# Kernel tuning notes

Hardware: AMD Instinct MI355X
Metric: run time of the kernel (lower is better)

Reference implementation:

```python
import jax, jax.numpy as jnp
import numpy as np

B = 128          # graphs per batch
NPG = 512        # nodes per graph
N = B * NPG      # 65536 nodes
E = 262144       # edges, avg degree 4, intra-graph only
IN_FEATS = 128
EDGE_FEATS = 32
EMB = 64
HEADS = 4
HC = EMB * HEADS  # 256
L = 3


def setup_inputs():
    ki = iter(jax.random.split(jax.random.key(0), 64))

    def nrm(shape):
        return jax.random.normal(next(ki), shape, jnp.float32)

    def lin(fan_in, shape):
        return jax.random.uniform(next(ki), shape, jnp.float32, -1.0, 1.0) / np.float32(np.sqrt(fan_in))

    x = nrm((N, IN_FEATS))
    edge_attr = nrm((E, EDGE_FEATS))
    g = jnp.arange(E) // (E // B)  # each edge stays inside its graph
    src = g * NPG + jax.random.randint(next(ki), (E,), 0, NPG)
    dst = g * NPG + jax.random.randint(next(ki), (E,), 0, NPG)
    edge_index = jnp.stack([src, dst]).astype(jnp.int32)
    batch_index = (jnp.arange(N) // NPG).astype(jnp.int32)
    d = dict(x=x, edge_attr=edge_attr, edge_index=edge_index, batch_index=batch_index)
    d['Wq1'] = lin(IN_FEATS, (IN_FEATS, HC)); d['bq1'] = lin(IN_FEATS, (HC,))
    d['Wk1'] = lin(IN_FEATS, (IN_FEATS, HC)); d['bk1'] = lin(IN_FEATS, (HC,))
    d['Wv1'] = lin(IN_FEATS, (IN_FEATS, HC)); d['bv1'] = lin(IN_FEATS, (HC,))
    d['We1'] = lin(EDGE_FEATS, (EDGE_FEATS, HC))
    d['Wskip1'] = lin(IN_FEATS, (IN_FEATS, HC)); d['bskip1'] = lin(IN_FEATS, (HC,))
    d['Wbeta1'] = lin(3 * HC, (3 * HC,))
    d['Wt1'] = lin(HC, (HC, EMB)); d['bt1'] = lin(HC, (EMB,))
    d['bng1'] = jnp.ones((EMB,), jnp.float32); d['bnb1'] = jnp.zeros((EMB,), jnp.float32)
    d['Wq'] = lin(EMB, (L, EMB, HC)); d['bq'] = lin(EMB, (L, HC))
    d['Wk'] = lin(EMB, (L, EMB, HC)); d['bk'] = lin(EMB, (L, HC))
    d['Wv'] = lin(EMB, (L, EMB, HC)); d['bv'] = lin(EMB, (L, HC))
    d['We'] = lin(EDGE_FEATS, (L, EDGE_FEATS, HC))
    d['Wskip'] = lin(EMB, (L, EMB, HC)); d['bskip'] = lin(EMB, (L, HC))
    d['Wbeta'] = lin(3 * HC, (L, 3 * HC))
    d['Wt'] = lin(HC, (L, HC, EMB)); d['bt'] = lin(HC, (L, EMB))
    d['bng'] = jnp.ones((L, EMB), jnp.float32); d['bnb'] = jnp.zeros((L, EMB), jnp.float32)
    d['pw0'] = lin(EMB, (EMB,)); d['pw2'] = lin(EMB, (EMB,))
    return d


def _tconv(x, src, dst, eattr, emask, Wq, bq, Wk, bk, Wv, bv, We, Wskip, bskip, Wbeta, n):
    # PyG TransformerConv (concat=True, beta=True, edge_dim), dropout off (eval)
    q = (x @ Wq + bq).reshape(n, HEADS, EMB)
    k = (x @ Wk + bk).reshape(n, HEADS, EMB)
    v = (x @ Wv + bv).reshape(n, HEADS, EMB)
    e = (eattr @ We).reshape(-1, HEADS, EMB)
    alpha = jnp.einsum('ehc,ehc->eh', q[dst], k[src] + e) / (EMB ** 0.5)
    alpha = jnp.where(emask[:, None], alpha, -jnp.inf)
    m = jax.ops.segment_max(alpha, dst, num_segments=n)
    m = jnp.where(jnp.isfinite(m), m, 0.0)
    p = jnp.where(emask[:, None], jnp.exp(alpha - m[dst]), 0.0)
    den = jax.ops.segment_sum(p, dst, num_segments=n)
    p = p / jnp.maximum(den, 1e-16)[dst]
    out = jax.ops.segment_sum((v[src] + e) * p[:, :, None], dst, num_segments=n).reshape(n, HC)
    xr = x @ Wskip + bskip
    beta = jax.nn.sigmoid(jnp.concatenate([out, xr, out - xr], axis=-1) @ Wbeta)[:, None]
    return beta * xr + (1.0 - beta) * out


def _bn(x, g, b):
    mu = x.mean(0)
    var = jnp.mean((x - mu) ** 2, 0)
    return (x - mu) / jnp.sqrt(var + 1e-5) * g + b


def _topk(x, src, dst, emask, w, npg, k_keep):
    # PyG TopKPooling: score = tanh(x.w / |w|), keep top ratio per graph, scale kept x by score
    n_graphs = x.shape[0] // npg
    score = jnp.tanh((x @ w) / jnp.linalg.norm(w))
    sv, idx = jax.lax.top_k(score.reshape(n_graphs, npg), k_keep)
    perm = (idx + jnp.arange(n_graphs)[:, None] * npg).reshape(-1)
    x_new = x[perm] * sv.reshape(-1)[:, None]
    new_idx = jnp.full(n_graphs * npg, -1, jnp.int32).at[perm].set(
        jnp.arange(n_graphs * k_keep, dtype=jnp.int32))
    sn, dn = new_idx[src], new_idx[dst]
    valid = emask & (sn >= 0) & (dn >= 0)
    return x_new, jnp.where(valid, sn, 0), jnp.where(valid, dn, 0), valid


def _forward(x, edge_attr, edge_index, batch_index, Wq1, bq1, Wk1, bk1, Wv1, bv1,
             We1, Wskip1, bskip1, Wbeta1, Wt1, bt1, bng1, bnb1,
             Wq, bq, Wk, bk, Wv, bv, We, Wskip, bskip, Wbeta, Wt, bt, bng, bnb,
             pw0, pw2):
    src, dst = edge_index[0], edge_index[1]
    emask = jnp.ones(src.shape, dtype=bool)
    n = x.shape[0]
    npg = n // B
    x = _tconv(x, src, dst, edge_attr, emask, Wq1, bq1, Wk1, bk1, Wv1, bv1,
               We1, Wskip1, bskip1, Wbeta1, n)
    x = _bn(jax.nn.relu(x @ Wt1 + bt1), bng1, bnb1)
    pool_w = {0: pw0, 2: pw2}
    greps = []
    for i in range(L):
        x = _tconv(x, src, dst, edge_attr, emask, Wq[i], bq[i], Wk[i], bk[i], Wv[i], bv[i],
                   We[i], Wskip[i], bskip[i], Wbeta[i], n)
        x = _bn(jax.nn.relu(x @ Wt[i] + bt[i]), bng[i], bnb[i])
        if i % 3 == 0 or i == L - 1:  # pooling at layers 0 and 2
            k_keep = npg // 2
            x, src, dst, emask = _topk(x, src, dst, emask, pool_w[i], npg, k_keep)
            npg = k_keep
            n = B * npg
            batch = jnp.arange(n) // npg  # pooled nodes stay contiguous per graph
            gmax = jax.ops.segment_max(x, batch, num_segments=B)
            gmean = jax.ops.segment_sum(x, batch, num_segments=B) / npg
            greps.append(jnp.concatenate([gmax, gmean], axis=-1))
    return greps[0] + greps[1]


def reference(x, edge_attr, edge_index, batch_index, Wq1, bq1, Wk1, bk1, Wv1, bv1,
              We1, Wskip1, bskip1, Wbeta1, Wt1, bt1, bng1, bnb1,
              Wq, bq, Wk, bk, Wv, bv, We, Wskip, bskip, Wbeta, Wt, bt, bng, bnb,
              pw0, pw2):
    return _forward(x, edge_attr, edge_index, batch_index, Wq1, bq1, Wk1, bk1, Wv1, bv1,
                    We1, Wskip1, bskip1, Wbeta1, Wt1, bt1, bng1, bnb1,
                    Wq, bq, Wk, bk, Wv, bv, We, Wskip, bskip, Wbeta, Wt, bt, bng, bnb,
                    pw0, pw2)
```

## Files before the change

### kernel.cpp

```cpp
#include <hip/hip_runtime.h>
#include <hip/hip_bf16.h>

#define NGRAPH 128
#define NTOT   65536
#define NE     262144
#define EPG    2048
#define HC     256

typedef __hip_bfloat16 bf16;

__device__ __forceinline__ float4 f4fma(float a, float4 b, float4 c){
  return make_float4(fmaf(a,b.x,c.x), fmaf(a,b.y,c.y), fmaf(a,b.z,c.z), fmaf(a,b.w,c.w));
}
__device__ __forceinline__ float4 f4add(float4 a, float4 b){
  return make_float4(a.x+b.x, a.y+b.y, a.z+b.z, a.w+b.w);
}

template<int F>
__global__ __launch_bounds__(256)
void gemm_qkvs_kernel(const float* __restrict__ X,
                      const float* __restrict__ W0, const float* __restrict__ B0,
                      const float* __restrict__ W1, const float* __restrict__ B1,
                      const float* __restrict__ W2, const float* __restrict__ B2,
                      const float* __restrict__ W3, const float* __restrict__ B3,
                      float* __restrict__ Y, long ystride)
{
  const int s = blockIdx.y;
  const float* __restrict__ W = (s==0)?W0:(s==1)?W1:(s==2)?W2:W3;
  const float* __restrict__ Bb= (s==0)?B0:(s==1)?B1:(s==2)?B2:B3;
  float* __restrict__ Yo = Y + (long)s*ystride;

  __shared__ __align__(16) float XsT[F][36];
  const int tid  = threadIdx.x;
  const int tcol = tid & 63;
  const int trow = tid >> 6;
  const long r0 = (long)blockIdx.x * 32;
  for (int idx = tid; idx < 32*F; idx += 256){
    int r = idx / F;
    int f = idx - r*F;
    XsT[f][r] = X[(r0 + r)*F + f];
  }
  __syncthreads();
  float4 acc[8];
#pragma unroll
  for (int r = 0; r < 8; ++r) acc[r] = make_float4(0.f,0.f,0.f,0.f);
  for (int f = 0; f < F; ++f){
    float4 w = *(const float4*)(&W[f*HC + 4*tcol]);
    float xs[8];
    *(float4*)&xs[0] = *(const float4*)(&XsT[f][8*trow]);
    *(float4*)&xs[4] = *(const float4*)(&XsT[f][8*trow + 4]);
#pragma unroll
    for (int r = 0; r < 8; ++r) acc[r] = f4fma(xs[r], w, acc[r]);
  }
  float4 bb = *(const float4*)(&Bb[4*tcol]);
#pragma unroll
  for (int r = 0; r < 8; ++r)
    *(float4*)(&Yo[(r0 + 8*trow + r)*HC + 4*tcol]) = f4add(acc[r], bb);
}

__global__ void mcomb_kernel(const float* __restrict__ Wq,
                             const float* __restrict__ bq,
                             const float* __restrict__ We,
                             int F, float* __restrict__ M)
{
  int id = blockIdx.x*256 + threadIdx.x;
  if (id >= (F+1)*128) return;
  int g = id >> 7;
  int j = id & 127;
  int h = j >> 5, f = j & 31;
  const float* row = (g < F) ? (Wq + (long)g*HC) : bq;
  const float* wr  = We + (long)f*HC + h*64;
  float s = 0.f;
#pragma unroll
  for (int c = 0; c < 64; ++c) s = fmaf(row[h*64 + c], wr[c], s);
  M[id] = s;
}

template<int F>
__global__ __launch_bounds__(256)
void qwe_gemm_kernel(const float* __restrict__ X, const float* __restrict__ M,
                     float* __restrict__ qwe)
{
  __shared__ __align__(16) float XsT[F][68];
  const int tid  = threadIdx.x;
  const int tcol = tid & 31;
  const int trow = tid >> 5;
  const long r0 = (long)blockIdx.x * 64;
  for (int idx = tid; idx < 64*F; idx += 256){
    int r = idx / F;
    int f = idx - r*F;
    XsT[f][r] = X[(r0 + r)*F + f];
  }
  __syncthreads();
  float4 acc[8];
#pragma unroll
  for (int r = 0; r < 8; ++r) acc[r] = make_float4(0.f,0.f,0.f,0.f);
  for (int f = 0; f < F; ++f){
    float4 w = *(const float4*)(&M[f*128 + 4*tcol]);
    float xs[8];
    *(float4*)&xs[0] = *(const float4*)(&XsT[f][8*trow]);
    *(float4*)&xs[4] = *(const float4*)(&XsT[f][8*trow + 4]);
#pragma unroll
    for (int r = 0; r < 8; ++r) acc[r] = f4fma(xs[r], w, acc[r]);
  }
  float4 bb = *(const float4*)(&M[F*128 + 4*tcol]);
#pragma unroll
  for (int r = 0; r < 8; ++r)
    *(float4*)(&qwe[(r0 + 8*trow + r)*128 + 4*tcol]) = f4add(acc[r], bb);
}

__global__ __launch_bounds__(256)
void csr_build_kernel(const int* __restrict__ dstA, int npgLoc,
                      int* __restrict__ eids, int* __restrict__ rowptr,
                      int* __restrict__ deg)
{
  __shared__ int dloc[2048];
  __shared__ int ord[2048];
  __shared__ int cnt[512];
  __shared__ int base[512];
  const int g = blockIdx.x, tid = threadIdx.x;
  const int ebase = g*2048;
  const int nbase = g*npgLoc;
  for (int e = tid; e < 2048; e += 256){
    int d = dstA[ebase + e];
    dloc[e] = (d >= 0) ? (d - nbase) : -1;
  }
  for (int d = tid; d < npgLoc; d += 256) cnt[d] = 0;
  __syncthreads();
  for (int r = 0; r < 8; ++r){
    const int e = r*256 + tid;
    const int d = dloc[e];
    int rk = -1;
    if (d >= 0){
      rk = cnt[d];
      for (int u = r*256; u < e; ++u)
        rk += (dloc[u] == d);
    }
    ord[e] = rk;
    __syncthreads();
    if (d >= 0) atomicAdd(&cnt[d], 1);
    __syncthreads();
  }
  if (tid == 0){
    int run = 0;
    for (int d = 0; d < npgLoc; ++d){ base[d] = run; run += cnt[d]; }
  }
  __syncthreads();
  for (int e = tid; e < 2048; e += 256){
    int d = dloc[e];
    if (d >= 0) eids[ebase + base[d] + ord[e]] = ebase + e;
  }
  for (int d = tid; d < npgLoc; d += 256){
    rowptr[nbase + d] = ebase + base[d];
    deg   [nbase + d] = cnt[d];
  }
}

__global__ __launch_bounds__(256)
void attn_kernel(int nodeOff,
                 const float* q, const float* __restrict__ k,
                 const float* __restrict__ v, const float* __restrict__ skip,
                 const float* __restrict__ qwe,
                 const int* __restrict__ rowptr, const int* __restrict__ deg,
                 const int* __restrict__ eids, const int* __restrict__ srcA,
                 const float* __restrict__ EA, const float* __restrict__ We,
                 const float* __restrict__ Wb, float* xout)
{
  const int lane = threadIdx.x & 63;
  const int h    = threadIdx.x >> 6;
  const int il   = blockIdx.x;
  const int i    = nodeOff + il;
  const int c    = h*64 + lane;

  const float qv = q[(long)il*HC + c];
  const float qw = (lane < 32) ? qwe[(long)il*128 + h*32 + lane] : 0.f;

  const int p0 = rowptr[i];
  const int dg = deg[i];
  int e_l = 0, s_l = 0;
  if (lane < dg){ e_l = eids[p0 + lane]; s_l = srcA[e_l] - nodeOff; }

  float m = -__builtin_inff();
  float den = 0.f, acc = 0.f, wsum = 0.f;

  for (int t = 0; t < dg; ++t){
    int e, s;
    if (t < 64){ e = __shfl(e_l, t); s = __shfl(s_l, t); }
    else { e = eids[p0 + t]; s = srcA[e] - nodeOff; }
    float ea = (lane < 32) ? EA[(long)e*32 + lane] : 0.f;
    float kk = k[(long)s*HC + c];
    float vv = v[(long)s*HC + c];
    float part = fmaf(qv, kk, ea*qw);
    part += __shfl_xor(part, 1);
    part += __shfl_xor(part, 2);
    part += __shfl_xor(part, 4);
    part += __shfl_xor(part, 8);
    part += __shfl_xor(part, 16);
    part += __shfl_xor(part, 32);
    float alpha = part * 0.125f;
    float nm  = fmaxf(m, alpha);
    float scl = __expf(m - nm);
    float p   = __expf(alpha - nm);
    den  = den*scl + p;
    acc  = fmaf(acc,  scl, p*vv);
    wsum = fmaf(wsum, scl, p*ea);
    m = nm;
  }

  float ecorr = 0.f;
#pragma unroll
  for (int f = 0; f < 32; ++f)
    ecorr = fmaf(__shfl(wsum, f), We[f*HC + c], ecorr);
  float inv = 1.f / fmaxf(den, 1e-16f);
  float o = (acc + ecorr) * inv;

  float xr = skip[(long)il*HC + c];
  float tp = o*Wb[c] + xr*Wb[HC + c] + (o - xr)*Wb[2*HC + c];
  tp += __shfl_xor(tp, 1);
  tp += __shfl_xor(tp, 2);
  tp += __shfl_xor(tp, 4);
  tp += __shfl_xor(tp, 8);
  tp += __shfl_xor(tp, 16);
  tp += __shfl_xor(tp, 32);
  __shared__ float tsh[4];
  if (lane == 0) tsh[h] = tp;
  __syncthreads();
  float tt = tsh[0] + tsh[1] + tsh[2] + tsh[3];
  float beta = 1.f / (1.f + __expf(-tt));
  xout[(long)il*HC + c] = beta*xr + (1.f - beta)*o;
}

__global__ __launch_bounds__(256)
void gemm_wt_kernel(const float* __restrict__ Xa, const float* __restrict__ Wt,
                    const float* __restrict__ bt, float* __restrict__ y)
{
  __shared__ __align__(16) float XsT[64][132];
  const int tid  = threadIdx.x;
  const int tcol = tid & 15;
  const int trow = tid >> 4;
  const long r0 = (long)blockIdx.x * 128;
  float4 acc[8];
#pragma unroll
  for (int r = 0; r < 8; ++r) acc[r] = make_float4(0.f,0.f,0.f,0.f);
  for (int kc = 0; kc < 4; ++kc){
    for (int idx = tid; idx < 128*64; idx += 256){
      int r = idx >> 6;
      int f = idx & 63;
      XsT[f][r] = Xa[(r0 + r)*HC + kc*64 + f];
    }
    __syncthreads();
    for (int f = 0; f < 64; ++f){
      float4 w = *(const float4*)(&Wt[(kc*64 + f)*64 + 4*tcol]);
      float xs[8];
      *(float4*)&xs[0] = *(const float4*)(&XsT[f][8*trow]);
      *(float4*)&xs[4] = *(const float4*)(&XsT[f][8*trow + 4]);
#pragma unroll
      for (int r = 0; r < 8; ++r) acc[r] = f4fma(xs[r], w, acc[r]);
    }
    __syncthreads();
  }
  float4 bb = *(const float4*)(&bt[4*tcol]);
#pragma unroll
  for (int r = 0; r < 8; ++r){
    float4 o = f4add(acc[r], bb);
    o.x = fmaxf(o.x, 0.f); o.y = fmaxf(o.y, 0.f);
    o.z = fmaxf(o.z, 0.f); o.w = fmaxf(o.w, 0.f);
    *(float4*)(&y[(r0 + 8*trow + r)*64 + 4*tcol]) = o;
  }
}

__global__ __launch_bounds__(256)
void bn_stats_kernel(const float* __restrict__ y, long total4,
                     float* __restrict__ psum, float* __restrict__ psq)
{
  __shared__ float s1[256][4], s2[256][4];
  const int tid = threadIdx.x;
  float a0=0,a1=0,a2=0,a3=0,b0=0,b1=0,b2=0,b3=0;
  const float4* y4 = (const float4*)y;
  for (long j = (long)blockIdx.x*256 + tid; j < total4; j += 65536){
    float4 v = y4[j];
    a0 += v.x; b0 += v.x*v.x;
    a1 += v.y; b1 += v.y*v.y;
    a2 += v.z; b2 += v.z*v.z;
    a3 += v.w; b3 += v.w*v.w;
  }
  s1[tid][0]=a0; s1[tid][1]=a1; s1[tid][2]=a2; s1[tid][3]=a3;
  s2[tid][0]=b0; s2[tid][1]=b1; s2[tid][2]=b2; s2[tid][3]=b3;
  __syncthreads();
  if (tid < 64){
    int t0 = tid >> 2, comp = tid & 3;
    float sa = 0.f, sb = 0.f;
#pragma unroll
    for (int kk = 0; kk < 16; ++kk){
      sa += s1[t0 + 16*kk][comp];
      sb += s2[t0 + 16*kk][comp];
    }
    psum[(long)blockIdx.x*64 + tid] = sa;
    psq [(long)blockIdx.x*64 + tid] = sb;
  }
}

__global__ void bn_finalize_kernel(const float* __restrict__ psum,
                                   const float* __restrict__ psq,
                                   float n_f, float* musd)
{
  __shared__ float s1[4][64], s2[4][64];
  const int col = threadIdx.x & 63;
  const int part = threadIdx.x >> 6;
  float a = 0.f, b = 0.f;
  for (int j = part; j < 256; j += 4){
    a += psum[(long)j*64 + col];
    b += psq [(long)j*64 + col];
  }
  s1[part][col] = a; s2[part][col] = b;
  __syncthreads();
  if (threadIdx.x < 64){
    int c = threadIdx.x;
    float sa = s1[0][c] + s1[1][c] + s1[2][c] + s1[3][c];
    float sb = s2[0][c] + s2[1][c] + s2[2][c] + s2[3][c];
    float mu = sa / n_f;
    float var = sb / n_f - mu*mu;
    musd[c] = mu;
    musd[64 + c] = rsqrtf(var + 1e-5f);
  }
}

__global__ void bn_apply_kernel(float* y, const float* __restrict__ musd,
                                const float* __restrict__ g,
                                const float* __restrict__ b, long total)
{
  long i4 = ((long)blockIdx.x * 256 + threadIdx.x) * 4;
  if (i4 >= total) return;
  int c0 = (int)(i4 & 63);
  float4 yv = *(float4*)&y[i4];
  yv.x = (yv.x - musd[c0+0]) * musd[64+c0+0] * g[c0+0] + b[c0+0];
  yv.y = (yv.y - musd[c0+1]) * musd[64+c0+1] * g[c0+1] + b[c0+1];
  yv.z = (yv.z - musd[c0+2]) * musd[64+c0+2] * g[c0+2] + b[c0+2];
  yv.w = (yv.w - musd[c0+3]) * musd[64+c0+3] * g[c0+3] + b[c0+3];
  *(float4*)&y[i4] = yv;
}

__global__ __launch_bounds__(256)
void topk_kernel(const float* __restrict__ x, const float* __restrict__ pw,
                 float* __restrict__ x2, int* __restrict__ newidx,
                 int npg, int kkeep)
{
  __shared__ float sc[512];
  __shared__ float wS[64];
  const int g = blockIdx.x, tid = threadIdx.x;
  if (tid < 64) wS[tid] = pw[tid];
  __syncthreads();
  float nrm = 0.f;
#pragma unroll
  for (int c = 0; c < 64; ++c) nrm += wS[c]*wS[c];
  nrm = sqrtf(nrm);
  for (int il = tid; il < npg; il += 256){
    const float* xr = x + (long)(g*npg + il)*64;
    float d = 0.f;
    for (int c = 0; c < 64; ++c) d = fmaf(xr[c], wS[c], d);
    sc[il] = tanhf(d / nrm);
  }
  __syncthreads();
  for (int il = tid; il < npg; il += 256){
    float si = sc[il];
    int r = 0;
    for (int j = 0; j < npg; ++j){
      float sj = sc[j];
      r += (sj > si) || (sj == si && j < il);
    }
    int gi = g*npg + il;
    if (r < kkeep){
      int npos = g*kkeep + r;
      newidx[gi] = npos;
      const float4* xr4 = (const float4*)(x + (long)gi*64);
      float4* xo4 = (float4*)(x2 + (long)npos*64);
#pragma unroll
      for (int c4 = 0; c4 < 16; ++c4){
        float4 xv = xr4[c4];
        xo4[c4] = make_float4(xv.x*si, xv.y*si, xv.z*si, xv.w*si);
      }
    } else {
      newidx[gi] = -1;
    }
  }
}

__global__ void remap_kernel(const int* __restrict__ src0, const int* __restrict__ dst0,
                             const int* __restrict__ newidx,
                             int* __restrict__ src2, int* __restrict__ dst2)
{
  int e = blockIdx.x * 256 + threadIdx.x;
  int ns = newidx[src0[e]];
  int nd = newidx[dst0[e]];
  bool ok = (ns >= 0) && (nd >= 0);
  src2[e] = ok ? ns : 0;
  dst2[e] = ok ? nd : -1;
}

__global__ void gpool_kernel(const float* __restrict__ x2, int kkeep,
                             float* grep0, float* out, int mode)
{
  const int g = blockIdx.x, c = threadIdx.x;
  float mx = -__builtin_inff(), s = 0.f;
  for (int j = 0; j < kkeep; ++j){
    float vv = x2[((long)g*kkeep + j)*64 + c];
    mx = fmaxf(mx, vv);
    s += vv;
  }
  float mean = s / (float)kkeep;
  if (mode == 0){
    grep0[g*128 + c] = mx;
    grep0[g*128 + 64 + c] = mean;
  } else {
    out[g*128 + c]      = grep0[g*128 + c] + mx;
    out[g*128 + 64 + c] = grep0[g*128 + 64 + c] + mean;
  }
}

extern "C" void kernel_launch(void* const* d_in, const int* in_sizes, int n_in,
                              void* d_out, int out_size, void* d_ws, size_t ws_size,
                              hipStream_t stream)
{
  const float* x_in = (const float*)d_in[0];
  const float* EA   = (const float*)d_in[1];
  const int*   eidx = (const int*)d_in[2];
  const int*   src0 = eidx;
  const int*   dst0 = eidx + NE;

  const float* Wq1    = (const float*)d_in[4];
  const float* bq1    = (const float*)d_in[5];
  const float* Wk1    = (const float*)d_in[6];
  const float* bk1    = (const float*)d_in[7];
  const float* Wv1    = (const float*)d_in[8];
  const float* bv1    = (const float*)d_in[9];
  const float* We1    = (const float*)d_in[10];
  const float* Wskip1 = (const float*)d_in[11];
  const float* bskip1 = (const float*)d_in[12];
  const float* Wbeta1 = (const float*)d_in[13];
  const float* Wt1    = (const float*)d_in[14];
  const float* bt1    = (const float*)d_in[15];
  const float* bng1   = (const float*)d_in[16];
  const float* bnb1   = (const float*)d_in[17];
  const float* WqL    = (const float*)d_in[18];
  const float* bqL    = (const float*)d_in[19];
  const float* WkL    = (const float*)d_in[20];
  const float* bkL    = (const float*)d_in[21];
  const float* WvL    = (const float*)d_in[22];
  const float* bvL    = (const float*)d_in[23];
  const float* WeL    = (const float*)d_in[24];
  const float* WskipL = (const float*)d_in[25];
  const float* bskipL = (const float*)d_in[26];
  const float* WbetaL = (const float*)d_in[27];
  const float* WtL    = (const float*)d_in[28];
  const float* btL    = (const float*)d_in[29];
  const float* bngL   = (const float*)d_in[30];
  const float* bnbL   = (const float*)d_in[31];
  const float* pw0    = (const float*)d_in[32];
  const float* pw2    = (const float*)d_in[33];

  const size_t FIXED = 33554432ull;
  int chunks = 1;
  while (chunks < 32 && 9ull*(67108864ull/chunks)/2 + FIXED > ws_size)
    chunks <<= 1;
  const int gpc = NGRAPH / chunks;
  const size_t C = 67108864ull / chunks;
  const long CF = (long)(C / 4);

  char* wsb = (char*)d_ws;
  float* qb   = (float*)(wsb);
  float* kb   = (float*)(wsb + C);
  float* vb   = (float*)(wsb + 2*C);
  float* sk   = (float*)(wsb + 3*C);
  float* qweb = (float*)(wsb + 4*C);
  char* p = wsb + 4*C + C/2;
  auto alloc = [&](size_t bytes){ char* r = p; p += (bytes + 255) & ~255ull; return r; };
  float* y      = (float*)alloc(16777216ull);
  float* x2     = (float*)alloc(8388608ull);
  float* ps     = (float*)alloc(65536ull);
  float* pq     = (float*)alloc(65536ull);
  float* musd   = (float*)alloc(4096ull);
  float* grep0  = (float*)alloc(65536ull);
  float* Mbuf   = (float*)alloc(66304ull);
  int* newidx   = (int*)alloc(262144ull);
  int* src2     = (int*)alloc(1048576ull);
  int* dst2     = (int*)alloc(1048576ull);
  int* eidsA    = (int*)alloc(1048576ull);
  int* rowptrA  = (int*)alloc(262144ull);
  int* degA     = (int*)alloc(262144ull);
  int* eidsB    = (int*)alloc(1048576ull);
  int* rowptrB  = (int*)alloc(131072ull);
  int* degB     = (int*)alloc(131072ull);

  csr_build_kernel<<<NGRAPH, 256, 0, stream>>>(dst0, 512, eidsA, rowptrA, degA);

  {
    const int npg = 512, n = NTOT;
    mcomb_kernel<<<(129*128 + 255)/256, 256, 0, stream>>>(Wq1, bq1, We1, 128, Mbuf);
    for (int c = 0; c < chunks; ++c){
      const int nOff = c * gpc * npg;
      const int nc   = gpc * npg;
      const float* Xc = x_in + (long)nOff * 128;
      dim3 grid(nc/32, 4);
      gemm_qkvs_kernel<128><<<grid, 256, 0, stream>>>(
          Xc, Wq1, bq1, Wk1, bk1, Wv1, bv1, Wskip1, bskip1, qb, CF);
      qwe_gemm_kernel<128><<<nc/64, 256, 0, stream>>>(Xc, Mbuf, qweb);
      attn_kernel<<<nc, 256, 0, stream>>>(nOff, qb, kb, vb, sk, qweb,
          rowptrA, degA, eidsA, src0, EA, We1, Wbeta1, qb);
      gemm_wt_kernel<<<nc/128, 256, 0, stream>>>(qb, Wt1, bt1, y + (long)nOff*64);
    }
    bn_stats_kernel<<<256, 256, 0, stream>>>(y, (long)n*16, ps, pq);
    bn_finalize_kernel<<<1, 256, 0, stream>>>(ps, pq, (float)n, musd);
    bn_apply_kernel<<<n/16, 256, 0, stream>>>(y, musd, bng1, bnb1, (long)n*64);
  }

  for (int i = 0; i < 3; ++i){
    const int n   = (i == 0) ? NTOT : NTOT/2;
    const int npg = (i == 0) ? 512 : 256;
    const float* xin = (i == 0) ? y : ((i == 1) ? x2 : y);
    const int* rp = (i == 0) ? rowptrA : rowptrB;
    const int* dgp= (i == 0) ? degA    : degB;
    const int* ei = (i == 0) ? eidsA   : eidsB;
    const int* sA = (i == 0) ? src0    : src2;
    const float* Wq_ = WqL + (long)i*64*256;  const float* bq_ = bqL + i*256;
    const float* Wk_ = WkL + (long)i*64*256;  const float* bk_ = bkL + i*256;
    const float* Wv_ = WvL + (long)i*64*256;  const float* bv_ = bvL + i*256;
    const float* Ws_ = WskipL + (long)i*64*256; const float* bs_ = bskipL + i*256;
    const float* We_ = WeL + (long)i*32*256;
    const float* Wb_ = WbetaL + i*768;
    const float* Wt_ = WtL + (long)i*256*64;  const float* bt_ = btL + i*64;
    const float* g_  = bngL + i*64;           const float* b_  = bnbL + i*64;

    mcomb_kernel<<<(65*128 + 255)/256, 256, 0, stream>>>(Wq_, bq_, We_, 64, Mbuf);
    for (int c = 0; c < chunks; ++c){
      const int nOff = c * gpc * npg;
      const int nc   = gpc * npg;
      const float* Xc = xin + (long)nOff * 64;
      dim3 grid(nc/32, 4);
      gemm_qkvs_kernel<64><<<grid, 256, 0, stream>>>(
          Xc, Wq_, bq_, Wk_, bk_, Wv_, bv_, Ws_, bs_, qb, CF);
      qwe_gemm_kernel<64><<<nc/64, 256, 0, stream>>>(Xc, Mbuf, qweb);
      attn_kernel<<<nc, 256, 0, stream>>>(nOff, qb, kb, vb, sk, qweb,
          rp, dgp, ei, sA, EA, We_, Wb_, qb);
      gemm_wt_kernel<<<nc/128, 256, 0, stream>>>(qb, Wt_, bt_, y + (long)nOff*64);
    }
    bn_stats_kernel<<<256, 256, 0, stream>>>(y, (long)n*16, ps, pq);
    bn_finalize_kernel<<<1, 256, 0, stream>>>(ps, pq, (float)n, musd);
    bn_apply_kernel<<<n/16, 256, 0, stream>>>(y, musd, g_, b_, (long)n*64);

    if (i == 0){
      topk_kernel<<<NGRAPH, 256, 0, stream>>>(y, pw0, x2, newidx, 512, 256);
      remap_kernel<<<NE/256, 256, 0, stream>>>(src0, dst0, newidx, src2, dst2);
      csr_build_kernel<<<NGRAPH, 256, 0, stream>>>(dst2, 256, eidsB, rowptrB, degB);
      gpool_kernel<<<NGRAPH, 64, 0, stream>>>(x2, 256, grep0, (float*)d_out, 0);
    } else if (i == 2){
      topk_kernel<<<NGRAPH, 256, 0, stream>>>(y, pw2, x2, newidx, 256, 128);
      gpool_kernel<<<NGRAPH, 64, 0, stream>>>(x2, 128, grep0, (float*)d_out, 1);
    }
  }

  (void)in_sizes; (void)n_in; (void)out_size; (void)ws_size;
}
```

Baseline: 1.833 ms.

## Process one node per wavefront in attention kernel with float4 channel loads

The attention kernel now assigns one destination node per 64-lane wavefront instead of one per 256-thread block. Each lane handles four contiguous channels through float4 loads of q, k, v, skip and We. The per-head dot-product reduction shrinks to four shuffle steps, and the cross-head shared-memory reduction and block barrier are removed. This cuts block count and per-edge shuffle work and uses wider memory transactions, at the cost of more registers per lane and a new lane-to-head and edge-feature mapping that must stay correct.

```diff
diff --git a/kernel.cpp b/kernel.cpp
--- a/kernel.cpp
+++ b/kernel.cpp
@@ -167,13 +167,12 @@
                  const float* __restrict__ Wb, float* xout)
 {
   const int lane = threadIdx.x & 63;
-  const int h    = threadIdx.x >> 6;
-  const int il   = blockIdx.x;
+  const int g16  = lane & 15;
+  const int il   = blockIdx.x*4 + (threadIdx.x >> 6);
   const int i    = nodeOff + il;
-  const int c    = h*64 + lane;
-
-  const float qv = q[(long)il*HC + c];
-  const float qw = (lane < 32) ? qwe[(long)il*128 + h*32 + lane] : 0.f;
+
+  float4 q4  = *(const float4*)(&q[(long)il*HC + 4*lane]);
+  float2 qw2 = *(const float2*)(&qwe[(long)il*128 + 2*lane]);
 
   const int p0 = rowptr[i];
   const int dg = deg[i];
@@ -181,53 +180,72 @@
   if (lane < dg){ e_l = eids[p0 + lane]; s_l = srcA[e_l] - nodeOff; }
 
   float m = -__builtin_inff();
-  float den = 0.f, acc = 0.f, wsum = 0.f;
+  float den = 0.f;
+  float4 acc = make_float4(0.f,0.f,0.f,0.f);
+  float2 wsum = make_float2(0.f,0.f);
 
   for (int t = 0; t < dg; ++t){
     int e, s;
     if (t < 64){ e = __shfl(e_l, t); s = __shfl(s_l, t); }
     else { e = eids[p0 + t]; s = srcA[e] - nodeOff; }
-    float ea = (lane < 32) ? EA[(long)e*32 + lane] : 0.f;
-    float kk = k[(long)s*HC + c];
-    float vv = v[(long)s*HC + c];
-    float part = fmaf(qv, kk, ea*qw);
+    float2 ea2 = *(const float2*)(&EA[(long)e*32 + 2*g16]);
+    float4 k4  = *(const float4*)(&k[(long)s*HC + 4*lane]);
+    float4 v4  = *(const float4*)(&v[(long)s*HC + 4*lane]);
+    float part = q4.x*k4.x + q4.y*k4.y + q4.z*k4.z + q4.w*k4.w
+               + qw2.x*ea2.x + qw2.y*ea2.y;
     part += __shfl_xor(part, 1);
     part += __shfl_xor(part, 2);
     part += __shfl_xor(part, 4);
     part += __shfl_xor(part, 8);
-    part += __shfl_xor(part, 16);
-    part += __shfl_xor(part, 32);
     float alpha = part * 0.125f;
     float nm  = fmaxf(m, alpha);
     float scl = __expf(m - nm);
     float p   = __expf(alpha - nm);
-    den  = den*scl + p;
-    acc  = fmaf(acc,  scl, p*vv);
-    wsum = fmaf(wsum, scl, p*ea);
+    den = den*scl + p;
+    acc.x = fmaf(acc.x, scl, p*v4.x);
+    acc.y = fmaf(acc.y, scl, p*v4.y);
+    acc.z = fmaf(acc.z, scl, p*v4.z);
+    acc.w = fmaf(acc.w, scl, p*v4.w);
+    wsum.x = fmaf(wsum.x, scl, p*ea2.x);
+    wsum.y = fmaf(wsum.y, scl, p*ea2.y);
     m = nm;
   }
 
-  float ecorr = 0.f;
-#pragma unroll
-  for (int f = 0; f < 32; ++f)
-    ecorr = fmaf(__shfl(wsum, f), We[f*HC + c], ecorr);
+  float4 ecorr = make_float4(0.f,0.f,0.f,0.f);
+#pragma unroll
+  for (int j = 0; j < 16; ++j){
+    int srcl = (lane & 48) | j;
+    float wx = __shfl(wsum.x, srcl);
+    float wy = __shfl(wsum.y, srcl);
+    float4 w0 = *(const float4*)(&We[(2*j)*HC + 4*lane]);
+    float4 w1 = *(const float4*)(&We[(2*j+1)*HC + 4*lane]);
+    ecorr = f4fma(wx, w0, ecorr);
+    ecorr = f4fma(wy, w1, ecorr);
+  }
   float inv = 1.f / fmaxf(den, 1e-16f);
-  float o = (acc + ecorr) * inv;
-
-  float xr = skip[(long)il*HC + c];
-  float tp = o*Wb[c] + xr*Wb[HC + c] + (o - xr)*Wb[2*HC + c];
+  float4 o = make_float4((acc.x+ecorr.x)*inv, (acc.y+ecorr.y)*inv,
+                         (acc.z+ecorr.z)*inv, (acc.w+ecorr.w)*inv);
+
+  float4 xr  = *(const float4*)(&skip[(long)il*HC + 4*lane]);
+  float4 wb1 = *(const float4*)(&Wb[4*lane]);
+  float4 wb2 = *(const float4*)(&Wb[HC + 4*lane]);
+  float4 wb3 = *(const float4*)(&Wb[2*HC + 4*lane]);
+  float tp = o.x*wb1.x + o.y*wb1.y + o.z*wb1.z + o.w*wb1.w
+           + xr.x*wb2.x + xr.y*wb2.y + xr.z*wb2.z + xr.w*wb2.w
+           + (o.x-xr.x)*wb3.x + (o.y-xr.y)*wb3.y
+           + (o.z-xr.z)*wb3.z + (o.w-xr.w)*wb3.w;
   tp += __shfl_xor(tp, 1);
   tp += __shfl_xor(tp, 2);
   tp += __shfl_xor(tp, 4);
   tp += __shfl_xor(tp, 8);
   tp += __shfl_xor(tp, 16);
   tp += __shfl_xor(tp, 32);
-  __shared__ float tsh[4];
-  if (lane == 0) tsh[h] = tp;
-  __syncthreads();
-  float tt = tsh[0] + tsh[1] + tsh[2] + tsh[3];
-  float beta = 1.f / (1.f + __expf(-tt));
-  xout[(long)il*HC + c] = beta*xr + (1.f - beta)*o;
+  float beta = 1.f / (1.f + __expf(-tp));
+  float4 xo = make_float4(beta*xr.x + (1.f-beta)*o.x,
+                          beta*xr.y + (1.f-beta)*o.y,
+                          beta*xr.z + (1.f-beta)*o.z,
+                          beta*xr.w + (1.f-beta)*o.w);
+  *(float4*)(&xout[(long)il*HC + 4*lane]) = xo;
 }
 
 __global__ __launch_bounds__(256)
@@ -504,7 +522,7 @@
       gemm_qkvs_kernel<128><<<grid, 256, 0, stream>>>(
           Xc, Wq1, bq1, Wk1, bk1, Wv1, bv1, Wskip1, bskip1, qb, CF);
       qwe_gemm_kernel<128><<<nc/64, 256, 0, stream>>>(Xc, Mbuf, qweb);
-      attn_kernel<<<nc, 256, 0, stream>>>(nOff, qb, kb, vb, sk, qweb,
+      attn_kernel<<<nc/4, 256, 0, stream>>>(nOff, qb, kb, vb, sk, qweb,
           rowptrA, degA, eidsA, src0, EA, We1, Wbeta1, qb);
       gemm_wt_kernel<<<nc/128, 256, 0, stream>>>(qb, Wt1, bt1, y + (long)nOff*64);
     }
@@ -539,7 +557,7 @@
       gemm_qkvs_kernel<64><<<grid, 256, 0, stream>>>(
           Xc, Wq_, bq_, Wk_, bk_, Wv_, bv_, Ws_, bs_, qb, CF);
       qwe_gemm_kernel<64><<<nc/64, 256, 0, stream>>>(Xc, Mbuf, qweb);
-      attn_kernel<<<nc, 256, 0, stream>>>(nOff, qb, kb, vb, sk, qweb,
+      attn_kernel<<<nc/4, 256, 0, stream>>>(nOff, qb, kb, vb, sk, qweb,
           rp, dgp, ei, sA, EA, We_, Wb_, qb);
       gemm_wt_kernel<<<nc/128, 256, 0, stream>>>(qb, Wt_, bt_, y + (long)nOff*64);
     }
```

Result: faster. 1.572 ms (-14.2%).
